# Optimization experiments

Measured on AMD Instinct MI355X. Metric: run time of the kernel, lower is better.

## Reference

```python
import jax, jax.numpy as jnp
import numpy as np

B, S, D = 2, 2048, 1024
H = 16
DK = D // H  # 64
NORM = 1.0 / np.sqrt(D / H)


def setup_inputs() -> dict:
    key = jax.random.key(0)
    ks = jax.random.split(key, 13)
    inp = {
        "q": jax.random.normal(ks[0], (B, S, D), jnp.float32),
        "k": jax.random.normal(ks[1], (B, S, D), jnp.float32),
        "v": jax.random.normal(ks[2], (B, S, D), jnp.float32),
        "attn_mask": jax.random.normal(ks[3], (B, 1, S, S), jnp.float32),
        "attn_mask1": jax.random.uniform(ks[4], (B, 1, S, S), jnp.float32),
        # torch Linear weights: [out, in], y = x @ W.T + b
        "wq_w": jax.random.normal(ks[5], (D, D), jnp.float32) * 0.02,
        "wq_b": jnp.zeros((D,), jnp.float32),
        "wk_w": jax.random.normal(ks[6], (D, D), jnp.float32) * 0.02,
        "wk_b": jnp.zeros((D,), jnp.float32),
        "wv_w": jax.random.normal(ks[7], (D, D), jnp.float32) * 0.02,
        "wv_b": jnp.zeros((D,), jnp.float32),
        "wo_w": jax.random.normal(ks[8], (D, D), jnp.float32) * 0.02,
        "wo_b": jnp.zeros((D,), jnp.float32),
    }
    return inp


def reference(q, k, v, attn_mask, attn_mask1,
              wq_w, wq_b, wk_w, wk_b, wv_w, wv_b, wo_w, wo_b):
    b = q.shape[0]
    Q = q @ wq_w.T + wq_b  # [B,S,D]
    K = k @ wk_w.T + wk_b
    V = v @ wv_w.T + wv_b
    # NOTE: original uses raw .reshape (not transpose) to split heads
    Q = Q.reshape(b, H, q.shape[1], DK)
    K = K.reshape(b, H, k.shape[1], DK)
    V = V.reshape(b, H, v.shape[1], DK)
    scores = jnp.einsum('bhqd,bhkd->bhqk', Q, K) * NORM
    attn = jax.nn.softmax(scores + attn_mask, axis=-1)
    attn = attn * attn_mask1  # post-softmax multiplicative mask
    val = jnp.einsum('bhqk,bhkd->bhqd', attn, V).reshape(b, Q.shape[2], -1)
    return val @ wo_w.T + wo_b
```

## Files before the change

kernel.cpp:

```cpp
#include <hip/hip_runtime.h>
#include <hip/hip_bf16.h>
#include <stdint.h>


typedef __bf16 bf16x8 __attribute__((ext_vector_type(8)));
typedef float f32x4 __attribute__((ext_vector_type(4)));

#define DEVI __device__ __forceinline__

static constexpr int S = 2048, D = 1024, H = 16, DK = 64, BATCH = 2;
static constexpr int BS = BATCH * S;

DEVI void gload_lds16(const void* g, void* l) {
  __builtin_amdgcn_global_load_lds((const __attribute__((address_space(1))) void*)g,
                                   (__attribute__((address_space(3))) void*)l, 16, 0, 0);
}

__global__ void cast_f32_to_bf16(const float* __restrict__ in, __bf16* __restrict__ out, int n) {
  int i = (blockIdx.x * blockDim.x + threadIdx.x) * 8;
  if (i >= n) return;
  float4 a = *(const float4*)(in + i);
  float4 b = *(const float4*)(in + i + 4);
  bf16x8 o;
  o[0] = (__bf16)a.x; o[1] = (__bf16)a.y; o[2] = (__bf16)a.z; o[3] = (__bf16)a.w;
  o[4] = (__bf16)b.x; o[5] = (__bf16)b.y; o[6] = (__bf16)b.z; o[7] = (__bf16)b.w;
  *(bf16x8*)(out + i) = o;
}

template <bool OUT_BF16>
__global__ void gemm_bt(const __bf16* __restrict__ A, const __bf16* __restrict__ W,
                        const float* __restrict__ bias, void* __restrict__ out,
                        float scale, int M, int N, int K) {
  __shared__ __bf16 As[128 * 64];
  __shared__ __bf16 Bs[128 * 64];
  const int t = threadIdx.x;
  const int w = t >> 6, l = t & 63;
  const int c = l & 15, g = l >> 4;
  const int wr = w >> 1, wc = w & 1;
  const int m0 = blockIdx.x * 128, n0 = blockIdx.y * 128;

  const int srow = (w << 3) + (l >> 3);
  const int scol = (l & 7) << 3;
  char* AsB = (char*)As;
  char* BsB = (char*)Bs;

  f32x4 acc[4][4] = {};

  for (int k0 = 0; k0 < K; k0 += 64) {
#pragma unroll
    for (int i = 0; i < 4; ++i) {
      int row = (i << 5) + srow;
      gload_lds16(A + (size_t)(m0 + row) * K + k0 + scol, AsB + (i << 12) + (w << 10));
      gload_lds16(W + (size_t)(n0 + row) * K + k0 + scol, BsB + (i << 12) + (w << 10));
    }
    __syncthreads();
#pragma unroll
    for (int kf = 0; kf < 2; ++kf) {
      bf16x8 a[4], b[4];
#pragma unroll
      for (int mi = 0; mi < 4; ++mi) {
        int rowA = (wr << 6) + (mi << 4) + c;
        int rowB = (wc << 6) + (mi << 4) + c;
        a[mi] = *(const bf16x8*)(AsB + rowA * 128 + (kf << 6) + (g << 4));
        b[mi] = *(const bf16x8*)(BsB + rowB * 128 + (kf << 6) + (g << 4));
      }
#pragma unroll
      for (int mi = 0; mi < 4; ++mi)
#pragma unroll
        for (int ni = 0; ni < 4; ++ni)
          acc[mi][ni] = __builtin_amdgcn_mfma_f32_16x16x32_bf16(a[mi], b[ni], acc[mi][ni], 0, 0, 0);
    }
    __syncthreads();
  }

#pragma unroll
  for (int ni = 0; ni < 4; ++ni) {
    int col = n0 + (wc << 6) + (ni << 4) + c;
    float bv = bias[col];
#pragma unroll
    for (int mi = 0; mi < 4; ++mi) {
#pragma unroll
      for (int r = 0; r < 4; ++r) {
        int row = m0 + (wr << 6) + (mi << 4) + (g << 2) + r;
        float v = (acc[mi][ni][r] + bv) * scale;
        if (OUT_BF16) ((__bf16*)out)[(size_t)row * N + col] = (__bf16)v;
        else          ((float*)out)[(size_t)row * N + col] = v;
      }
    }
  }
}

__global__ void attn_fused(const __bf16* __restrict__ Qb, const __bf16* __restrict__ Kb,
                           const __bf16* __restrict__ Vb, const float* __restrict__ mask,
                           const float* __restrict__ mask1, __bf16* __restrict__ outb) {
  __shared__ __bf16 Ks[4][32 * 64];
  __shared__ __bf16 Vs[4][32 * 64];
  __shared__ __bf16 Ps[4][16 * 40];

  const int t = threadIdx.x, w = t >> 6, l = t & 63;
  const int c = l & 15, g = l >> 4;
  const int q0 = blockIdx.x << 4;
  const int h = (blockIdx.y << 2) + w;
  const int b = blockIdx.z;
  const size_t bh = (size_t)b * H + h;
  const __bf16* Qh = Qb + bh * S * DK;
  const __bf16* Kh = Kb + bh * S * DK;
  const __bf16* Vh = Vb + bh * S * DK;
  const float* mk_base = mask + (size_t)b * S * S;
  const float* m1_base = mask1 + (size_t)b * S * S;

  bf16x8 qf0 = *(const bf16x8*)(Qh + (q0 + c) * DK + (g << 3));
  bf16x8 qf1 = *(const bf16x8*)(Qh + (q0 + c) * DK + 32 + (g << 3));

  const int krow = l >> 3;
  const int kcol = (l & 7) << 3;

  char* KsB = (char*)&Ks[w][0];
  char* VsB = (char*)&Vs[w][0];
  const __bf16* Vsp = &Vs[w][0];

  float mrun[4] = {-1e30f, -1e30f, -1e30f, -1e30f};
  float lrun[4] = {0.f, 0.f, 0.f, 0.f};
  f32x4 acc[4] = {};

  for (int k0 = 0; k0 < S; k0 += 32) {
#pragma unroll
    for (int i = 0; i < 4; ++i) {
      gload_lds16(Kh + (size_t)(k0 + (i << 3) + krow) * DK + kcol, KsB + (i << 10));
      gload_lds16(Vh + (size_t)(k0 + (i << 3) + krow) * DK + kcol, VsB + (i << 10));
    }
    float mk[2][4], m1[2][4];
#pragma unroll
    for (int kt = 0; kt < 2; ++kt)
#pragma unroll
      for (int r = 0; r < 4; ++r) {
        size_t idx = (size_t)(q0 + (g << 2) + r) * S + (size_t)(k0 + (kt << 4) + c);
        mk[kt][r] = mk_base[idx];
        m1[kt][r] = m1_base[idx];
      }
    __syncthreads();

    f32x4 sc[2];
#pragma unroll
    for (int kt = 0; kt < 2; ++kt) {
      int row = (kt << 4) + c;
      bf16x8 kf0 = *(const bf16x8*)(KsB + row * 128 + (g << 4));
      bf16x8 kf1 = *(const bf16x8*)(KsB + row * 128 + 64 + (g << 4));
      f32x4 z = {};
      z = __builtin_amdgcn_mfma_f32_16x16x32_bf16(qf0, kf0, z, 0, 0, 0);
      z = __builtin_amdgcn_mfma_f32_16x16x32_bf16(qf1, kf1, z, 0, 0, 0);
      sc[kt] = z;
    }

    float alpha[4];
#pragma unroll
    for (int r = 0; r < 4; ++r) {
      float l0 = sc[0][r] + mk[0][r];
      float l1 = sc[1][r] + mk[1][r];
      float mx = fmaxf(l0, l1);
      mx = fmaxf(mx, __shfl_xor(mx, 1));
      mx = fmaxf(mx, __shfl_xor(mx, 2));
      mx = fmaxf(mx, __shfl_xor(mx, 4));
      mx = fmaxf(mx, __shfl_xor(mx, 8));
      float mnew = fmaxf(mrun[r], mx);
      float al = __expf(mrun[r] - mnew);
      mrun[r] = mnew;
      alpha[r] = al;
      float p0 = __expf(l0 - mnew);
      float p1 = __expf(l1 - mnew);
      float rs = p0 + p1;
      rs += __shfl_xor(rs, 1);
      rs += __shfl_xor(rs, 2);
      rs += __shfl_xor(rs, 4);
      rs += __shfl_xor(rs, 8);
      lrun[r] = lrun[r] * al + rs;
      Ps[w][((g << 2) + r) * 40 + c] = (__bf16)(p0 * m1[0][r]);
      Ps[w][((g << 2) + r) * 40 + 16 + c] = (__bf16)(p1 * m1[1][r]);
    }
#pragma unroll
    for (int ni = 0; ni < 4; ++ni) {
      acc[ni][0] *= alpha[0];
      acc[ni][1] *= alpha[1];
      acc[ni][2] *= alpha[2];
      acc[ni][3] *= alpha[3];
    }

    bf16x8 pf = *(const bf16x8*)&Ps[w][c * 40 + (g << 3)];
    const __bf16* Vrow = Vsp + (g << 9) + c;
#pragma unroll
    for (int ni = 0; ni < 4; ++ni) {
      bf16x8 vf;
#pragma unroll
      for (int j = 0; j < 8; ++j) vf[j] = Vrow[(j << 6) + (ni << 4)];
      acc[ni] = __builtin_amdgcn_mfma_f32_16x16x32_bf16(pf, vf, acc[ni], 0, 0, 0);
    }
  }

  float inv[4];
#pragma unroll
  for (int r = 0; r < 4; ++r) inv[r] = 1.0f / lrun[r];
  __bf16* oh = outb + bh * S * DK;
#pragma unroll
  for (int ni = 0; ni < 4; ++ni)
#pragma unroll
    for (int r = 0; r < 4; ++r)
      oh[(size_t)(q0 + (g << 2) + r) * DK + (ni << 4) + c] = (__bf16)(acc[ni][r] * inv[r]);
}

extern "C" void kernel_launch(void* const* d_in, const int* in_sizes, int n_in,
                              void* d_out, int out_size, void* d_ws, size_t ws_size,
                              hipStream_t stream) {
  (void)in_sizes; (void)n_in; (void)out_size; (void)ws_size;
  const float* q   = (const float*)d_in[0];
  const float* k   = (const float*)d_in[1];
  const float* v   = (const float*)d_in[2];
  const float* am  = (const float*)d_in[3];
  const float* am1 = (const float*)d_in[4];
  const float* wq  = (const float*)d_in[5];
  const float* bq  = (const float*)d_in[6];
  const float* wk  = (const float*)d_in[7];
  const float* bk  = (const float*)d_in[8];
  const float* wv  = (const float*)d_in[9];
  const float* bv  = (const float*)d_in[10];
  const float* wo  = (const float*)d_in[11];
  const float* bo  = (const float*)d_in[12];

  const size_t NX = (size_t)BS * D;
  const size_t NW = (size_t)D * D;
  char* ws = (char*)d_ws;
  __bf16* xbf = (__bf16*)ws;
  __bf16* wb  = xbf + NX;
  __bf16* Qp  = wb + NW;
  __bf16* Kp  = Qp + NX;
  __bf16* Vp  = Kp + NX;
  __bf16* Vl  = xbf;

  auto cast = [&](const float* src, __bf16* dst, size_t n) {
    cast_f32_to_bf16<<<(int)(n / 8 / 256), 256, 0, stream>>>(src, dst, (int)n);
  };

  dim3 gg(BS / 128, D / 128);
  const float NORM = 0.125f;

  cast(q, xbf, NX);
  cast(wq, wb, NW);
  gemm_bt<true><<<gg, 256, 0, stream>>>(xbf, wb, bq, Qp, NORM, BS, D, D);
  cast(k, xbf, NX);
  cast(wk, wb, NW);
  gemm_bt<true><<<gg, 256, 0, stream>>>(xbf, wb, bk, Kp, 1.0f, BS, D, D);
  cast(v, xbf, NX);
  cast(wv, wb, NW);
  gemm_bt<true><<<gg, 256, 0, stream>>>(xbf, wb, bv, Vp, 1.0f, BS, D, D);

  dim3 ga(S / 16, H / 4, BATCH);
  attn_fused<<<ga, 256, 0, stream>>>(Qp, Kp, Vp, am, am1, Vl);

  cast(wo, wb, NW);
  gemm_bt<false><<<gg, 256, 0, stream>>>(Vl, wb, bo, d_out, 1.0f, BS, D, D);
}
```

Measured before the change: 502.8 us.

## Batch casts and QKV GEMMs, transpose V, and load attention K/V from global directly

Merges the seven separate cast launches into two batched cast kernels and the three projection GEMMs into one launch with 512-thread blocks covering 24 column tiles. The V projection is written transposed per head, so the attention kernel can load V fragments as contiguous 16-byte vectors. The attention kernel now reads K and V fragments straight from global memory into registers, which removes the per-tile LDS staging, the block barrier and the strided scalar V gathers. It also places bf16 staging buffers in the output buffer, and the transposed V stores in the GEMM epilogue are scattered.

```diff
diff --git a/kernel.cpp b/kernel.cpp
--- a/kernel.cpp
+++ b/kernel.cpp
@@ -16,9 +16,7 @@
                                    (__attribute__((address_space(3))) void*)l, 16, 0, 0);
 }
 
-__global__ void cast_f32_to_bf16(const float* __restrict__ in, __bf16* __restrict__ out, int n) {
-  int i = (blockIdx.x * blockDim.x + threadIdx.x) * 8;
-  if (i >= n) return;
+DEVI void cast8(const float* in, __bf16* out, int i) {
   float4 a = *(const float4*)(in + i);
   float4 b = *(const float4*)(in + i + 4);
   bf16x8 o;
@@ -27,74 +25,160 @@
   *(bf16x8*)(out + i) = o;
 }
 
-template <bool OUT_BF16>
-__global__ void gemm_bt(const __bf16* __restrict__ A, const __bf16* __restrict__ W,
-                        const float* __restrict__ bias, void* __restrict__ out,
-                        float scale, int M, int N, int K) {
+__global__ void cast3(const float* s0, const float* s1, const float* s2,
+                      __bf16* d0, __bf16* d1, __bf16* d2) {
+  int seg = blockIdx.x >> 11;
+  int i = (((blockIdx.x & 2047) << 8) + threadIdx.x) << 3;
+  const float* s = seg == 0 ? s0 : seg == 1 ? s1 : s2;
+  __bf16* d = seg == 0 ? d0 : seg == 1 ? d1 : d2;
+  cast8(s, d, i);
+}
+
+__global__ void cast4(const float* s0, const float* s1, const float* s2, const float* s3,
+                      __bf16* d0, __bf16* d1, __bf16* d2, __bf16* d3) {
+  int seg = blockIdx.x >> 9;
+  int i = (((blockIdx.x & 511) << 8) + threadIdx.x) << 3;
+  const float* s = seg == 0 ? s0 : seg == 1 ? s1 : seg == 2 ? s2 : s3;
+  __bf16* d = seg == 0 ? d0 : seg == 1 ? d1 : seg == 2 ? d2 : d3;
+  cast8(s, d, i);
+}
+
+__global__ __launch_bounds__(512)
+void gemm_qkv(const __bf16* __restrict__ xq, const __bf16* __restrict__ xk,
+              const __bf16* __restrict__ xv, const __bf16* __restrict__ wqb,
+              const __bf16* __restrict__ wkb, const __bf16* __restrict__ wvb,
+              const float* __restrict__ bq, const float* __restrict__ bk,
+              const float* __restrict__ bv, __bf16* __restrict__ Qp,
+              __bf16* __restrict__ Kp, __bf16* __restrict__ Vt) {
   __shared__ __bf16 As[128 * 64];
   __shared__ __bf16 Bs[128 * 64];
-  const int t = threadIdx.x;
-  const int w = t >> 6, l = t & 63;
-  const int c = l & 15, g = l >> 4;
-  const int wr = w >> 1, wc = w & 1;
-  const int m0 = blockIdx.x * 128, n0 = blockIdx.y * 128;
-
-  const int srow = (w << 3) + (l >> 3);
-  const int scol = (l & 7) << 3;
+  const int t = threadIdx.x, w = t >> 6;
+  const int l = t & 63, c = l & 15, g = l >> 4;
+  const int wr = w >> 2, wc = w & 3;
+  const int m0 = blockIdx.x * 128;
+  const int seg = blockIdx.y >> 3;
+  const int n0 = (blockIdx.y & 7) * 128;
+  const __bf16* A = seg == 0 ? xq : seg == 1 ? xk : xv;
+  const __bf16* W = seg == 0 ? wqb : seg == 1 ? wkb : wvb;
+  const float* bias = seg == 0 ? bq : seg == 1 ? bk : bv;
+
+  const int srow = t >> 3;
+  const int scol = (t & 7) << 3;
   char* AsB = (char*)As;
   char* BsB = (char*)Bs;
 
-  f32x4 acc[4][4] = {};
-
-  for (int k0 = 0; k0 < K; k0 += 64) {
-#pragma unroll
-    for (int i = 0; i < 4; ++i) {
-      int row = (i << 5) + srow;
-      gload_lds16(A + (size_t)(m0 + row) * K + k0 + scol, AsB + (i << 12) + (w << 10));
-      gload_lds16(W + (size_t)(n0 + row) * K + k0 + scol, BsB + (i << 12) + (w << 10));
+  f32x4 acc[4][2] = {};
+
+  for (int k0 = 0; k0 < D; k0 += 64) {
+#pragma unroll
+    for (int i = 0; i < 2; ++i) {
+      gload_lds16(A + (size_t)(m0 + (i << 6) + srow) * D + k0 + scol, AsB + (i << 13) + (w << 10));
+      gload_lds16(W + (size_t)(n0 + (i << 6) + srow) * D + k0 + scol, BsB + (i << 13) + (w << 10));
     }
     __syncthreads();
 #pragma unroll
     for (int kf = 0; kf < 2; ++kf) {
-      bf16x8 a[4], b[4];
-#pragma unroll
-      for (int mi = 0; mi < 4; ++mi) {
-        int rowA = (wr << 6) + (mi << 4) + c;
-        int rowB = (wc << 6) + (mi << 4) + c;
-        a[mi] = *(const bf16x8*)(AsB + rowA * 128 + (kf << 6) + (g << 4));
-        b[mi] = *(const bf16x8*)(BsB + rowB * 128 + (kf << 6) + (g << 4));
+      bf16x8 a[4], b[2];
+#pragma unroll
+      for (int mi = 0; mi < 4; ++mi)
+        a[mi] = *(const bf16x8*)(AsB + ((wr << 6) + (mi << 4) + c) * 128 + (kf << 6) + (g << 4));
+#pragma unroll
+      for (int ni = 0; ni < 2; ++ni)
+        b[ni] = *(const bf16x8*)(BsB + ((wc << 5) + (ni << 4) + c) * 128 + (kf << 6) + (g << 4));
+#pragma unroll
+      for (int mi = 0; mi < 4; ++mi)
+#pragma unroll
+        for (int ni = 0; ni < 2; ++ni)
+          acc[mi][ni] = __builtin_amdgcn_mfma_f32_16x16x32_bf16(a[mi], b[ni], acc[mi][ni], 0, 0, 0);
+    }
+    __syncthreads();
+  }
+
+  const float scale = (seg == 0) ? 0.125f : 1.0f;
+#pragma unroll
+  for (int ni = 0; ni < 2; ++ni) {
+    const int col = n0 + (wc << 5) + (ni << 4) + c;
+    const float bvv = bias[col];
+#pragma unroll
+    for (int mi = 0; mi < 4; ++mi) {
+#pragma unroll
+      for (int r = 0; r < 4; ++r) {
+        const int row = m0 + (wr << 6) + (mi << 4) + (g << 2) + r;
+        const float v = (acc[mi][ni][r] + bvv) * scale;
+        if (seg < 2) {
+          __bf16* out = seg == 0 ? Qp : Kp;
+          out[(size_t)row * D + col] = (__bf16)v;
+        } else {
+          const int so = row & 2047;
+          const int b_ = row >> 11;
+          const int h_ = so >> 7;
+          const int s2 = ((so & 127) << 4) + (col >> 6);
+          const int dk = col & 63;
+          Vt[(((size_t)(b_ * H + h_) << 6) + dk) * S + s2] = (__bf16)v;
+        }
       }
+    }
+  }
+}
+
+__global__ __launch_bounds__(512)
+void gemm_out(const __bf16* __restrict__ A, const __bf16* __restrict__ W,
+              const float* __restrict__ bias, float* __restrict__ out) {
+  __shared__ __bf16 As[128 * 64];
+  __shared__ __bf16 Bs[128 * 64];
+  const int t = threadIdx.x, w = t >> 6;
+  const int l = t & 63, c = l & 15, g = l >> 4;
+  const int wr = w >> 2, wc = w & 3;
+  const int m0 = blockIdx.x * 128, n0 = blockIdx.y * 128;
+  const int srow = t >> 3;
+  const int scol = (t & 7) << 3;
+  char* AsB = (char*)As;
+  char* BsB = (char*)Bs;
+
+  f32x4 acc[4][2] = {};
+
+  for (int k0 = 0; k0 < D; k0 += 64) {
+#pragma unroll
+    for (int i = 0; i < 2; ++i) {
+      gload_lds16(A + (size_t)(m0 + (i << 6) + srow) * D + k0 + scol, AsB + (i << 13) + (w << 10));
+      gload_lds16(W + (size_t)(n0 + (i << 6) + srow) * D + k0 + scol, BsB + (i << 13) + (w << 10));
+    }
+    __syncthreads();
+#pragma unroll
+    for (int kf = 0; kf < 2; ++kf) {
+      bf16x8 a[4], b[2];
 #pragma unroll
       for (int mi = 0; mi < 4; ++mi)
-#pragma unroll
-        for (int ni = 0; ni < 4; ++ni)
+        a[mi] = *(const bf16x8*)(AsB + ((wr << 6) + (mi << 4) + c) * 128 + (kf << 6) + (g << 4));
+#pragma unroll
+      for (int ni = 0; ni < 2; ++ni)
+        b[ni] = *(const bf16x8*)(BsB + ((wc << 5) + (ni << 4) + c) * 128 + (kf << 6) + (g << 4));
+#pragma unroll
+      for (int mi = 0; mi < 4; ++mi)
+#pragma unroll
+        for (int ni = 0; ni < 2; ++ni)
           acc[mi][ni] = __builtin_amdgcn_mfma_f32_16x16x32_bf16(a[mi], b[ni], acc[mi][ni], 0, 0, 0);
     }
     __syncthreads();
   }
 
 #pragma unroll
-  for (int ni = 0; ni < 4; ++ni) {
-    int col = n0 + (wc << 6) + (ni << 4) + c;
-    float bv = bias[col];
-#pragma unroll
-    for (int mi = 0; mi < 4; ++mi) {
+  for (int ni = 0; ni < 2; ++ni) {
+    const int col = n0 + (wc << 5) + (ni << 4) + c;
+    const float bvv = bias[col];
+#pragma unroll
+    for (int mi = 0; mi < 4; ++mi)
 #pragma unroll
       for (int r = 0; r < 4; ++r) {
-        int row = m0 + (wr << 6) + (mi << 4) + (g << 2) + r;
-        float v = (acc[mi][ni][r] + bv) * scale;
-        if (OUT_BF16) ((__bf16*)out)[(size_t)row * N + col] = (__bf16)v;
-        else          ((float*)out)[(size_t)row * N + col] = v;
+        const int row = m0 + (wr << 6) + (mi << 4) + (g << 2) + r;
+        out[(size_t)row * D + col] = acc[mi][ni][r] + bvv;
       }
-    }
-  }
-}
-
-__global__ void attn_fused(const __bf16* __restrict__ Qb, const __bf16* __restrict__ Kb,
-                           const __bf16* __restrict__ Vb, const float* __restrict__ mask,
+  }
+}
+
+__global__ void attn_fused(const __bf16* __restrict__ Qp, const __bf16* __restrict__ Kp,
+                           const __bf16* __restrict__ Vt, const float* __restrict__ mask,
                            const float* __restrict__ mask1, __bf16* __restrict__ outb) {
-  __shared__ __bf16 Ks[4][32 * 64];
-  __shared__ __bf16 Vs[4][32 * 64];
   __shared__ __bf16 Ps[4][16 * 40];
 
   const int t = threadIdx.x, w = t >> 6, l = t & 63;
@@ -103,32 +187,30 @@
   const int h = (blockIdx.y << 2) + w;
   const int b = blockIdx.z;
   const size_t bh = (size_t)b * H + h;
-  const __bf16* Qh = Qb + bh * S * DK;
-  const __bf16* Kh = Kb + bh * S * DK;
-  const __bf16* Vh = Vb + bh * S * DK;
+  const __bf16* Qh = Qp + bh * S * DK;
+  const __bf16* Kh = Kp + bh * S * DK;
+  const __bf16* Vth = Vt + bh * DK * S;
   const float* mk_base = mask + (size_t)b * S * S;
   const float* m1_base = mask1 + (size_t)b * S * S;
 
-  bf16x8 qf0 = *(const bf16x8*)(Qh + (q0 + c) * DK + (g << 3));
-  bf16x8 qf1 = *(const bf16x8*)(Qh + (q0 + c) * DK + 32 + (g << 3));
-
-  const int krow = l >> 3;
-  const int kcol = (l & 7) << 3;
-
-  char* KsB = (char*)&Ks[w][0];
-  char* VsB = (char*)&Vs[w][0];
-  const __bf16* Vsp = &Vs[w][0];
+  const bf16x8 qf0 = *(const bf16x8*)(Qh + (q0 + c) * DK + (g << 3));
+  const bf16x8 qf1 = *(const bf16x8*)(Qh + (q0 + c) * DK + 32 + (g << 3));
 
   float mrun[4] = {-1e30f, -1e30f, -1e30f, -1e30f};
   float lrun[4] = {0.f, 0.f, 0.f, 0.f};
   f32x4 acc[4] = {};
 
   for (int k0 = 0; k0 < S; k0 += 32) {
-#pragma unroll
-    for (int i = 0; i < 4; ++i) {
-      gload_lds16(Kh + (size_t)(k0 + (i << 3) + krow) * DK + kcol, KsB + (i << 10));
-      gload_lds16(Vh + (size_t)(k0 + (i << 3) + krow) * DK + kcol, VsB + (i << 10));
-    }
+    bf16x8 kfr[2][2];
+#pragma unroll
+    for (int kt = 0; kt < 2; ++kt)
+#pragma unroll
+      for (int hf = 0; hf < 2; ++hf)
+        kfr[kt][hf] = *(const bf16x8*)(Kh + (size_t)(k0 + (kt << 4) + c) * DK + (hf << 5) + (g << 3));
+    bf16x8 vfr[4];
+#pragma unroll
+    for (int ni = 0; ni < 4; ++ni)
+      vfr[ni] = *(const bf16x8*)(Vth + (size_t)((ni << 4) + c) * S + k0 + (g << 3));
     float mk[2][4], m1[2][4];
 #pragma unroll
     for (int kt = 0; kt < 2; ++kt)
@@ -138,17 +220,13 @@
         mk[kt][r] = mk_base[idx];
         m1[kt][r] = m1_base[idx];
       }
-    __syncthreads();
 
     f32x4 sc[2];
 #pragma unroll
     for (int kt = 0; kt < 2; ++kt) {
-      int row = (kt << 4) + c;
-      bf16x8 kf0 = *(const bf16x8*)(KsB + row * 128 + (g << 4));
-      bf16x8 kf1 = *(const bf16x8*)(KsB + row * 128 + 64 + (g << 4));
       f32x4 z = {};
-      z = __builtin_amdgcn_mfma_f32_16x16x32_bf16(qf0, kf0, z, 0, 0, 0);
-      z = __builtin_amdgcn_mfma_f32_16x16x32_bf16(qf1, kf1, z, 0, 0, 0);
+      z = __builtin_amdgcn_mfma_f32_16x16x32_bf16(qf0, kfr[kt][0], z, 0, 0, 0);
+      z = __builtin_amdgcn_mfma_f32_16x16x32_bf16(qf1, kfr[kt][1], z, 0, 0, 0);
       sc[kt] = z;
     }
 
@@ -185,15 +263,10 @@
       acc[ni][3] *= alpha[3];
     }
 
-    bf16x8 pf = *(const bf16x8*)&Ps[w][c * 40 + (g << 3)];
-    const __bf16* Vrow = Vsp + (g << 9) + c;
-#pragma unroll
-    for (int ni = 0; ni < 4; ++ni) {
-      bf16x8 vf;
-#pragma unroll
-      for (int j = 0; j < 8; ++j) vf[j] = Vrow[(j << 6) + (ni << 4)];
-      acc[ni] = __builtin_amdgcn_mfma_f32_16x16x32_bf16(pf, vf, acc[ni], 0, 0, 0);
-    }
+    const bf16x8 pf = *(const bf16x8*)&Ps[w][c * 40 + (g << 3)];
+#pragma unroll
+    for (int ni = 0; ni < 4; ++ni)
+      acc[ni] = __builtin_amdgcn_mfma_f32_16x16x32_bf16(pf, vfr[ni], acc[ni], 0, 0, 0);
   }
 
   float inv[4];
@@ -227,34 +300,29 @@
 
   const size_t NX = (size_t)BS * D;
   const size_t NW = (size_t)D * D;
+
+  __bf16* xq = (__bf16*)d_out;
+  __bf16* xk = xq + NX;
   char* ws = (char*)d_ws;
-  __bf16* xbf = (__bf16*)ws;
-  __bf16* wb  = xbf + NX;
-  __bf16* Qp  = wb + NW;
+  __bf16* xv  = (__bf16*)ws;
+  __bf16* wqb = xv + NX;
+  __bf16* wkb = wqb + NW;
+  __bf16* wvb = wkb + NW;
+  __bf16* wob = wvb + NW;
+  __bf16* Qp  = wob + NW;
   __bf16* Kp  = Qp + NX;
-  __bf16* Vp  = Kp + NX;
-  __bf16* Vl  = xbf;
-
-  auto cast = [&](const float* src, __bf16* dst, size_t n) {
-    cast_f32_to_bf16<<<(int)(n / 8 / 256), 256, 0, stream>>>(src, dst, (int)n);
-  };
-
-  dim3 gg(BS / 128, D / 128);
-  const float NORM = 0.125f;
-
-  cast(q, xbf, NX);
-  cast(wq, wb, NW);
-  gemm_bt<true><<<gg, 256, 0, stream>>>(xbf, wb, bq, Qp, NORM, BS, D, D);
-  cast(k, xbf, NX);
-  cast(wk, wb, NW);
-  gemm_bt<true><<<gg, 256, 0, stream>>>(xbf, wb, bk, Kp, 1.0f, BS, D, D);
-  cast(v, xbf, NX);
-  cast(wv, wb, NW);
-  gemm_bt<true><<<gg, 256, 0, stream>>>(xbf, wb, bv, Vp, 1.0f, BS, D, D);
+  __bf16* Vt  = Kp + NX;
+  __bf16* Vl  = xv;
+
+  cast3<<<3 * 2048, 256, 0, stream>>>(q, k, v, xq, xk, xv);
+  cast4<<<4 * 512, 256, 0, stream>>>(wq, wk, wv, wo, wqb, wkb, wvb, wob);
+
+  dim3 gq(BS / 128, 24);
+  gemm_qkv<<<gq, 512, 0, stream>>>(xq, xk, xv, wqb, wkb, wvb, bq, bk, bv, Qp, Kp, Vt);
 
   dim3 ga(S / 16, H / 4, BATCH);
-  attn_fused<<<ga, 256, 0, stream>>>(Qp, Kp, Vp, am, am1, Vl);
-
-  cast(wo, wb, NW);
-  gemm_bt<false><<<gg, 256, 0, stream>>>(Vl, wb, bo, d_out, 1.0f, BS, D, D);
-}
+  attn_fused<<<ga, 256, 0, stream>>>(Qp, Kp, Vt, am, am1, Vl);
+
+  dim3 go(BS / 128, D / 128);
+  gemm_out<<<go, 512, 0, stream>>>(Vl, wob, bo, (float*)d_out);
+}
```

New measurement: 517.6 us. 2.9% more time.
